# Kernel tuning notes

Hardware: AMD Instinct MI355X
Metric: run time of the kernel (lower is better)

Reference implementation:

```python
import jax, jax.numpy as jnp
import numpy as np

N_NODES = 100000
N_EDGES = 1600000
D_IN = 128
D_HID = 128
N_CLASS = 10
N_GRAPHS = 512
BN_EPS = 1e-5


def setup_inputs() -> dict:
    key = jax.random.key(0)
    ks = jax.random.split(key, 12)
    x = jax.random.normal(ks[0], (N_NODES, D_IN), dtype=jnp.float32)
    edge_index = jax.random.randint(ks[1], (2, N_EDGES), 0, N_NODES, dtype=jnp.int32)
    idx = jnp.sort(jax.random.randint(ks[2], (N_NODES,), 0, N_GRAPHS, dtype=jnp.int32))
    s = 1.0 / np.sqrt(D_HID)
    W1 = jax.random.uniform(ks[3], (D_IN, D_HID), minval=-s, maxval=s, dtype=jnp.float32)
    b1 = jnp.zeros((D_HID,), jnp.float32)
    W2 = jax.random.uniform(ks[4], (D_HID, D_HID), minval=-s, maxval=s, dtype=jnp.float32)
    b2 = jnp.zeros((D_HID,), jnp.float32)
    W3 = jax.random.uniform(ks[5], (D_HID, D_HID), minval=-s, maxval=s, dtype=jnp.float32)
    b3 = jnp.zeros((D_HID,), jnp.float32)
    W4 = jax.random.uniform(ks[6], (D_HID, N_CLASS), minval=-s, maxval=s, dtype=jnp.float32)
    b4 = jnp.zeros((N_CLASS,), jnp.float32)
    gamma = jnp.ones((D_HID,), jnp.float32)
    beta = jnp.zeros((D_HID,), jnp.float32)
    return {"x": x, "edge_index": edge_index, "idx": idx,
            "W1": W1, "b1": b1, "W2": W2, "b2": b2,
            "W3": W3, "b3": b3, "W4": W4, "b4": b4,
            "gamma": gamma, "beta": beta}


def _agg(h, src, dst):
    # (adj + I) @ h : sum of neighbor features plus self-loop
    return jax.ops.segment_sum(h[src], dst, num_segments=N_NODES) + h


def reference(x, edge_index, idx, W1, b1, W2, b2, W3, b3, W4, b4, gamma, beta):
    src, dst = edge_index[0], edge_index[1]
    z1 = jax.nn.relu(_agg(x, src, dst) @ W1 + b1)          # [N, H] (dropout = identity, eval)
    h = _agg(z1, src, dst) @ W2 + b2                        # [N, H]
    pooled = jax.ops.segment_sum(h, idx, num_segments=N_GRAPHS)  # [G, H] scatter-add readout
    # BatchNorm1d over graph (batch) dimension, training-mode batch stats
    mean = jnp.mean(pooled, axis=0)
    var = jnp.var(pooled, axis=0)
    out = (pooled - mean) * jax.lax.rsqrt(var + BN_EPS) * gamma + beta
    zg = jax.nn.relu(out @ W3 + b3)
    logits = zg @ W4 + b4                                   # [G, C]
    return jax.nn.log_softmax(logits, axis=1)
```

## Files before the change

kernel.cpp:

```cpp
#include <hip/hip_runtime.h>
#include <hip/hip_fp16.h>
#include <math.h>

#define NN 100000
#define NE 1600000
#define DH 128
#define NG 512
#define NC 10
#define NSEG 8
#define SEGN 12500
#define CHE 8192
#define NCH 196
#define MAXDEG 48
#define WPITCH 136

#define NB_HIST (NCH * NSEG)
#define NB_CNT  98
#define NB_GEMM ((NN + 63) / 64)

typedef __attribute__((ext_vector_type(8))) _Float16 f16x8;
typedef __attribute__((ext_vector_type(4))) float f32x4;


__global__ __launch_bounds__(256, 3) void k_build(
    const int* __restrict__ dst, const int* __restrict__ src,
    int* __restrict__ counts, int* __restrict__ csr,
    const int* __restrict__ gidx, int* __restrict__ cnt,
    const float* __restrict__ A, const float* __restrict__ W,
    __half* __restrict__ out) {
    int b = blockIdx.x;
    int t = threadIdx.x;
    if (b < NB_HIST) {
        int seg = b & 7;
        int chunk = b >> 3;
        int lo = seg * SEGN, hi = lo + SEGN;
        int e0 = chunk * CHE;
        int e1 = e0 + CHE < NE ? e0 + CHE : NE;
        for (int e = e0 + t * 4; e < e1; e += 1024) {
            int4 d4 = *(const int4*)(dst + e);
            bool i0 = d4.x >= lo && d4.x < hi;
            bool i1 = d4.y >= lo && d4.y < hi;
            bool i2 = d4.z >= lo && d4.z < hi;
            bool i3 = d4.w >= lo && d4.w < hi;
            int4 s4 = {0, 0, 0, 0};
            if (i0 | i1 | i2 | i3) s4 = *(const int4*)(src + e);
            if (i0) {
                int p = atomicAdd(&counts[d4.x], 1);
                if (p < MAXDEG) csr[d4.x * MAXDEG + p] = s4.x;
            }
            if (i1) {
                int p = atomicAdd(&counts[d4.y], 1);
                if (p < MAXDEG) csr[d4.y * MAXDEG + p] = s4.y;
            }
            if (i2) {
                int p = atomicAdd(&counts[d4.z], 1);
                if (p < MAXDEG) csr[d4.z * MAXDEG + p] = s4.z;
            }
            if (i3) {
                int p = atomicAdd(&counts[d4.w], 1);
                if (p < MAXDEG) csr[d4.w * MAXDEG + p] = s4.w;
            }
        }
    } else if (b < NB_HIST + NB_CNT) {
        int cb = b - NB_HIST;
        int n0 = cb * 1024 + t * 4;
        if (n0 >= NN) return;
        int g = gidx[n0];
        int run = 1;
        for (int j = 1; j < 4; ++j) {
            int n = n0 + j;
            if (n < NN) {
                int gg = gidx[n];
                if (gg == g) {
                    run++;
                } else {
                    atomicAdd(&cnt[g], run);
                    g = gg;
                    run = 1;
                }
            }
        }
        atomicAdd(&cnt[g], run);
    } else {
        __shared__ _Float16 sWT[DH * WPITCH];
        __shared__ __align__(16) _Float16 sOut[4][16][DH];
        int gb = b - (NB_HIST + NB_CNT);
        int wv = t >> 6;
        int lane = t & 63;
        for (int i = t; i < DH * DH; i += 256) {
            int k = i >> 7, n = i & 127;
            sWT[n * WPITCH + k] = (_Float16)W[i];
        }
        __syncthreads();

        int m = lane & 15;
        int quad = lane >> 4;
        int node0 = gb * 64 + wv * 16;
        int nodeA = node0 + m;
        if (nodeA >= NN) nodeA = NN - 1;
        const float* arow = A + (size_t)nodeA * DH;

        f16x8 afrag[4];
#pragma unroll
        for (int kt = 0; kt < 4; ++kt) {
            int k0 = kt * 32 + quad * 8;
            float4 u0 = *(const float4*)(arow + k0);
            float4 u1 = *(const float4*)(arow + k0 + 4);
            afrag[kt][0] = (_Float16)u0.x; afrag[kt][1] = (_Float16)u0.y;
            afrag[kt][2] = (_Float16)u0.z; afrag[kt][3] = (_Float16)u0.w;
            afrag[kt][4] = (_Float16)u1.x; afrag[kt][5] = (_Float16)u1.y;
            afrag[kt][6] = (_Float16)u1.z; afrag[kt][7] = (_Float16)u1.w;
        }

#pragma unroll
        for (int ct = 0; ct < 8; ++ct) {
            f32x4 acc = {0.f, 0.f, 0.f, 0.f};
            int n = ct * 16 + m;
#pragma unroll
            for (int kt = 0; kt < 4; ++kt) {
                int k0 = kt * 32 + quad * 8;
                f16x8 bfrag = *(const f16x8*)&sWT[n * WPITCH + k0];
                acc = __builtin_amdgcn_mfma_f32_16x16x32_f16(afrag[kt], bfrag, acc, 0, 0, 0);
            }
#pragma unroll
            for (int r = 0; r < 4; ++r)
                sOut[wv][quad * 4 + r][ct * 16 + m] = (_Float16)acc[r];
        }
        __syncthreads();

        const uint4* so = (const uint4*)&sOut[wv][0][0];
        for (int i = lane; i < 256; i += 64) {
            int row = i >> 4;
            int node = node0 + row;
            if (node < NN) ((uint4*)out)[(size_t)node * 16 + (i & 15)] = so[i];
        }
    }
}


__device__ __forceinline__ void acc8(float* a, const uint4& v, float m) {
    float2 f;
    f = __half22float2(*(const __half2*)&v.x); a[0] = fmaf(m, f.x, a[0]); a[1] = fmaf(m, f.y, a[1]);
    f = __half22float2(*(const __half2*)&v.y); a[2] = fmaf(m, f.x, a[2]); a[3] = fmaf(m, f.y, a[3]);
    f = __half22float2(*(const __half2*)&v.z); a[4] = fmaf(m, f.x, a[4]); a[5] = fmaf(m, f.y, a[5]);
    f = __half22float2(*(const __half2*)&v.w); a[6] = fmaf(m, f.x, a[6]); a[7] = fmaf(m, f.y, a[7]);
}


__global__ __launch_bounds__(256, 4) void k_agg_h(
    const __half* __restrict__ in, const int* __restrict__ counts,
    const int* __restrict__ csr, const float* __restrict__ bias,
    __half* __restrict__ outA) {
    int t = threadIdx.x;
    int lane = t & 15;
    int node = blockIdx.x * 16 + (t >> 4);
    const uint4* in4 = (const uint4*)in;
    float a[8];
#pragma unroll
    for (int j = 0; j < 8; ++j) a[j] = 0.f;
    uint4 sv = in4[(size_t)node * 16 + lane];
    acc8(a, sv, 1.f);
    int e0 = node * MAXDEG;
    int deg = counts[node];
    deg = deg < MAXDEG ? deg : MAXDEG;
    int e1 = e0 + deg;
    int elast = e1 - 1;
    for (int e = e0; e < e1; e += 8) {
        int idx[8];
        float m[8];
#pragma unroll
        for (int i = 0; i < 8; ++i) {
            int ei = e + i;
            int ec = ei < elast ? ei : elast;
            idx[i] = csr[ec];
            m[i] = (ei < e1) ? 1.f : 0.f;
        }
        uint4 v[8];
#pragma unroll
        for (int i = 0; i < 8; ++i) v[i] = in4[(size_t)idx[i] * 16 + lane];
#pragma unroll
        for (int i = 0; i < 8; ++i) acc8(a, v[i], m[i]);
    }
    float4 b0 = ((const float4*)bias)[lane * 2];
    float4 b1v = ((const float4*)bias)[lane * 2 + 1];
    a[0] = fmaxf(a[0] + b0.x, 0.f);  a[1] = fmaxf(a[1] + b0.y, 0.f);
    a[2] = fmaxf(a[2] + b0.z, 0.f);  a[3] = fmaxf(a[3] + b0.w, 0.f);
    a[4] = fmaxf(a[4] + b1v.x, 0.f); a[5] = fmaxf(a[5] + b1v.y, 0.f);
    a[6] = fmaxf(a[6] + b1v.z, 0.f); a[7] = fmaxf(a[7] + b1v.w, 0.f);
    uint4 o;
    *(__half2*)&o.x = __floats2half2_rn(a[0], a[1]);
    *(__half2*)&o.y = __floats2half2_rn(a[2], a[3]);
    *(__half2*)&o.z = __floats2half2_rn(a[4], a[5]);
    *(__half2*)&o.w = __floats2half2_rn(a[6], a[7]);
    ((uint4*)outA)[(size_t)node * 16 + lane] = o;
}


__global__ __launch_bounds__(256, 4) void k_agg_pool_h(
    const __half* __restrict__ in, const int* __restrict__ counts,
    const int* __restrict__ csr, const int* __restrict__ gidx,
    float* __restrict__ pp8) {
    __shared__ __align__(16) float sA[16][DH];
    int t = threadIdx.x;
    int lane = t & 15;
    int p = t >> 4;
    int node0 = blockIdx.x * 16;
    int node = node0 + p;
    const uint4* in4 = (const uint4*)in;
    float a[8];
#pragma unroll
    for (int j = 0; j < 8; ++j) a[j] = 0.f;
    uint4 sv = in4[(size_t)node * 16 + lane];
    acc8(a, sv, 1.f);
    int e0 = node * MAXDEG;
    int deg = counts[node];
    deg = deg < MAXDEG ? deg : MAXDEG;
    int e1 = e0 + deg;
    int elast = e1 - 1;
    for (int e = e0; e < e1; e += 8) {
        int idx[8];
        float m[8];
#pragma unroll
        for (int i = 0; i < 8; ++i) {
            int ei = e + i;
            int ec = ei < elast ? ei : elast;
            idx[i] = csr[ec];
            m[i] = (ei < e1) ? 1.f : 0.f;
        }
        uint4 v[8];
#pragma unroll
        for (int i = 0; i < 8; ++i) v[i] = in4[(size_t)idx[i] * 16 + lane];
#pragma unroll
        for (int i = 0; i < 8; ++i) acc8(a, v[i], m[i]);
    }
    float4* row = (float4*)&sA[p][lane * 8];
    row[0] = make_float4(a[0], a[1], a[2], a[3]);
    row[1] = make_float4(a[4], a[5], a[6], a[7]);
    __syncthreads();
    if (t < DH) {
        float* pp = pp8 + (size_t)(blockIdx.x & 7) * NG * DH;
        int gprev = gidx[node0];
        float run = 0.f;
        for (int q = 0; q < 16; ++q) {
            int g = gidx[node0 + q];
            if (g != gprev) {
                atomicAdd(&pp[gprev * DH + t], run);
                run = 0.f;
                gprev = g;
            }
            run += sA[q][t];
        }
        atomicAdd(&pp[gprev * DH + t], run);
    }
}


__device__ __forceinline__ void fma4(float4& acc, float s, const float4& wv) {
    acc.x = fmaf(s, wv.x, acc.x);
    acc.y = fmaf(s, wv.y, acc.y);
    acc.z = fmaf(s, wv.z, acc.z);
    acc.w = fmaf(s, wv.w, acc.w);
}


__global__ __launch_bounds__(256, 2) void k_pool_mm(
    const float* __restrict__ pp8, const float* __restrict__ W,
    const float* __restrict__ bias, const int* __restrict__ cnt,
    float* __restrict__ pooled) {
    __shared__ __align__(16) float sW[DH * DH];
    __shared__ __align__(16) float sA[32 * DH];
    int t = threadIdx.x;
    int g0 = blockIdx.x * 32;
    {
        const float4* W4g = (const float4*)W;
        float4* sW4 = (float4*)sW;
        for (int i = t; i < DH * DH / 4; i += 256) sW4[i] = W4g[i];
        const float4* P4 = (const float4*)pp8;
        float4* sA4 = (float4*)sA;
        for (int i = t; i < 32 * DH / 4; i += 256) {
            float4 s;
            s.x = 0.f; s.y = 0.f; s.z = 0.f; s.w = 0.f;
#pragma unroll
            for (int c = 0; c < NSEG; ++c) {
                float4 v = P4[(size_t)c * NG * DH / 4 + (size_t)g0 * DH / 4 + i];
                s.x += v.x; s.y += v.y; s.z += v.z; s.w += v.w;
            }
            sA4[i] = s;
        }
    }
    __syncthreads();

    int c4 = t & 31;
    int n0 = (t >> 5) * 4;
    const float4* sA4 = (const float4*)sA;
    const float4* sW4 = (const float4*)sW;
    float4 acc0, acc1, acc2, acc3;
    acc0.x = acc0.y = acc0.z = acc0.w = 0.f;
    acc1 = acc0; acc2 = acc0; acc3 = acc0;

#pragma unroll 2
    for (int kc = 0; kc < DH / 4; ++kc) {
        float4 a0 = sA4[(n0 + 0) * 32 + kc];
        float4 a1 = sA4[(n0 + 1) * 32 + kc];
        float4 a2 = sA4[(n0 + 2) * 32 + kc];
        float4 a3 = sA4[(n0 + 3) * 32 + kc];
        float4 w0 = sW4[(4 * kc + 0) * 32 + c4];
        float4 w1 = sW4[(4 * kc + 1) * 32 + c4];
        float4 w2 = sW4[(4 * kc + 2) * 32 + c4];
        float4 w3 = sW4[(4 * kc + 3) * 32 + c4];
        fma4(acc0, a0.x, w0); fma4(acc0, a0.y, w1); fma4(acc0, a0.z, w2); fma4(acc0, a0.w, w3);
        fma4(acc1, a1.x, w0); fma4(acc1, a1.y, w1); fma4(acc1, a1.z, w2); fma4(acc1, a1.w, w3);
        fma4(acc2, a2.x, w0); fma4(acc2, a2.y, w1); fma4(acc2, a2.z, w2); fma4(acc2, a2.w, w3);
        fma4(acc3, a3.x, w0); fma4(acc3, a3.y, w1); fma4(acc3, a3.z, w2); fma4(acc3, a3.w, w3);
    }

    float4 b2v = ((const float4*)bias)[c4];
    float c0 = (float)cnt[g0 + n0 + 0];
    float c1 = (float)cnt[g0 + n0 + 1];
    float c2 = (float)cnt[g0 + n0 + 2];
    float c3 = (float)cnt[g0 + n0 + 3];
    fma4(acc0, c0, b2v);
    fma4(acc1, c1, b2v);
    fma4(acc2, c2, b2v);
    fma4(acc3, c3, b2v);

    float4* out4 = (float4*)pooled;
    out4[(size_t)(g0 + n0 + 0) * 32 + c4] = acc0;
    out4[(size_t)(g0 + n0 + 1) * 32 + c4] = acc1;
    out4[(size_t)(g0 + n0 + 2) * 32 + c4] = acc2;
    out4[(size_t)(g0 + n0 + 3) * 32 + c4] = acc3;
}


__global__ void k_bnstats(const float* __restrict__ pooled, float* __restrict__ mean,
                          float* __restrict__ rstd) {
    int c = blockIdx.x;
    int l = threadIdx.x;
    float s = 0.f, s2 = 0.f;
    for (int g = l; g < NG; g += 64) {
        float v = pooled[g * DH + c];
        s += v;
        s2 += v * v;
    }
#pragma unroll
    for (int off = 32; off > 0; off >>= 1) {
        s += __shfl_down(s, off, 64);
        s2 += __shfl_down(s2, off, 64);
    }
    if (l == 0) {
        float m = s * (1.f / NG);
        float var = s2 * (1.f / NG) - m * m;
        mean[c] = m;
        rstd[c] = rsqrtf(var + 1e-5f);
    }
}


__global__ __launch_bounds__(128) void k_tail(
    const float* __restrict__ pooled, const float* __restrict__ mean,
    const float* __restrict__ rstd, const float* __restrict__ gamma,
    const float* __restrict__ beta, const float* __restrict__ W3,
    const float* __restrict__ b3, const float* __restrict__ W4,
    const float* __restrict__ b4, float* __restrict__ out) {
    __shared__ __align__(16) float sW[DH * DH];
    __shared__ float sg[DH];
    __shared__ float sz[DH];
    __shared__ float slog[NC];
    __shared__ float slse;
    int g = blockIdx.x, t = threadIdx.x;
    {
        const float4* W34 = (const float4*)W3;
        float4* sW4 = (float4*)sW;
        for (int i = t; i < DH * DH / 4; i += 128) sW4[i] = W34[i];
    }
    float v = pooled[g * DH + t];
    v = (v - mean[t]) * rstd[t] * gamma[t] + beta[t];
    sg[t] = v;
    __syncthreads();
    float acc = b3[t];
#pragma unroll 4
    for (int k = 0; k < DH; ++k) acc = fmaf(sg[k], sW[k * DH + t], acc);
    sz[t] = fmaxf(acc, 0.f);
    __syncthreads();
    if (t < NC) {
        float a = b4[t];
        for (int k = 0; k < DH; ++k) a = fmaf(sz[k], W4[k * NC + t], a);
        slog[t] = a;
    }
    __syncthreads();
    if (t == 0) {
        float mx = slog[0];
        for (int j = 1; j < NC; ++j) mx = fmaxf(mx, slog[j]);
        float se = 0.f;
        for (int j = 0; j < NC; ++j) se += expf(slog[j] - mx);
        slse = mx + logf(se);
    }
    __syncthreads();
    if (t < NC) out[g * NC + t] = slog[t] - slse;
}


extern "C" void kernel_launch(void* const* d_in, const int* in_sizes, int n_in,
                              void* d_out, int out_size, void* d_ws, size_t ws_size,
                              hipStream_t stream) {
    const float* x = (const float*)d_in[0];
    const int* ei = (const int*)d_in[1];
    const int* src = ei;
    const int* dst = ei + NE;
    const int* gidx = (const int*)d_in[2];
    const float* W1 = (const float*)d_in[3];
    const float* b1 = (const float*)d_in[4];
    const float* W2 = (const float*)d_in[5];
    const float* b2 = (const float*)d_in[6];
    const float* W3 = (const float*)d_in[7];
    const float* b3 = (const float*)d_in[8];
    const float* W4 = (const float*)d_in[9];
    const float* b4 = (const float*)d_in[10];
    const float* gamma = (const float*)d_in[11];
    const float* beta = (const float*)d_in[12];
    float* out = (float*)d_out;

    char* w = (char*)d_ws;
    auto take = [&](size_t bytes) {
        char* p = w;
        w += (bytes + 255) & ~size_t(255);
        return p;
    };
    int* counts = (int*)take((size_t)NN * 4);
    int* cnt = (int*)take((size_t)NG * 4);
    float* pp8 = (float*)take((size_t)NSEG * NG * DH * 4);
    size_t zero_bytes = (size_t)((char*)(pp8 + (size_t)NSEG * NG * DH) - (char*)counts);
    int* csr = (int*)take((size_t)NN * MAXDEG * 4);
    __half* y = (__half*)take((size_t)NN * DH * 2);
    __half* z1 = (__half*)take((size_t)NN * DH * 2);
    float* pooled = (float*)take((size_t)NG * DH * 4);
    float* meanb = (float*)take(DH * 4);
    float* rstdb = (float*)take(DH * 4);

    hipMemsetAsync(counts, 0, zero_bytes, stream);

    k_build<<<NB_HIST + NB_CNT + NB_GEMM, 256, 0, stream>>>(
        dst, src, counts, csr, gidx, cnt, x, W1, y);

    k_agg_h<<<NN / 16, 256, 0, stream>>>(y, counts, csr, b1, z1);

    k_agg_pool_h<<<NN / 16, 256, 0, stream>>>(z1, counts, csr, gidx, pp8);
    k_pool_mm<<<NG / 32, 256, 0, stream>>>(pp8, W2, b2, cnt, pooled);

    k_bnstats<<<DH, 64, 0, stream>>>(pooled, meanb, rstdb);
    k_tail<<<NG, 128, 0, stream>>>(pooled, meanb, rstdb, gamma, beta, W3, b3, W4, b4, out);
}
```

Baseline: 360.9 us.

## Store GEMM output in permuted column layout, swizzle weight LDS, drop sOut staging

The first-layer GEMM in k_build now keeps eight accumulators per wave and writes each lane's results straight to global memory in a permuted column order, which removes the sOut LDS staging buffer and its barrier. The permutation is undone downstream: the bias read in k_agg_h is reindexed and the rows of W2 are permuted when k_pool_mm loads them. The transposed weight tile in LDS uses an XOR swizzle instead of padding to avoid bank conflicts. Edge and activation reads use nontemporal loads, and the occupancy hint for k_build is raised, which risks register pressure.

```diff
diff --git a/kernel.cpp b/kernel.cpp
--- a/kernel.cpp
+++ b/kernel.cpp
@@ -12,17 +12,18 @@
 #define CHE 8192
 #define NCH 196
 #define MAXDEG 48
-#define WPITCH 136
 
 #define NB_HIST (NCH * NSEG)
 #define NB_CNT  98
 #define NB_GEMM ((NN + 63) / 64)
 
+
 typedef __attribute__((ext_vector_type(8))) _Float16 f16x8;
 typedef __attribute__((ext_vector_type(4))) float f32x4;
-
-
-__global__ __launch_bounds__(256, 3) void k_build(
+typedef __attribute__((ext_vector_type(4))) int i32x4;
+
+
+__global__ __launch_bounds__(256, 4) void k_build(
     const int* __restrict__ dst, const int* __restrict__ src,
     int* __restrict__ counts, int* __restrict__ csr,
     const int* __restrict__ gidx, int* __restrict__ cnt,
@@ -37,13 +38,14 @@
         int e0 = chunk * CHE;
         int e1 = e0 + CHE < NE ? e0 + CHE : NE;
         for (int e = e0 + t * 4; e < e1; e += 1024) {
-            int4 d4 = *(const int4*)(dst + e);
+            i32x4 d4 = __builtin_nontemporal_load((const i32x4*)(dst + e));
             bool i0 = d4.x >= lo && d4.x < hi;
             bool i1 = d4.y >= lo && d4.y < hi;
             bool i2 = d4.z >= lo && d4.z < hi;
             bool i3 = d4.w >= lo && d4.w < hi;
-            int4 s4 = {0, 0, 0, 0};
-            if (i0 | i1 | i2 | i3) s4 = *(const int4*)(src + e);
+            i32x4 s4 = {0, 0, 0, 0};
+            if (i0 | i1 | i2 | i3)
+                s4 = __builtin_nontemporal_load((const i32x4*)(src + e));
             if (i0) {
                 int p = atomicAdd(&counts[d4.x], 1);
                 if (p < MAXDEG) csr[d4.x * MAXDEG + p] = s4.x;
@@ -82,14 +84,13 @@
         }
         atomicAdd(&cnt[g], run);
     } else {
-        __shared__ _Float16 sWT[DH * WPITCH];
-        __shared__ __align__(16) _Float16 sOut[4][16][DH];
+        __shared__ _Float16 sWT[DH * 128];
         int gb = b - (NB_HIST + NB_CNT);
         int wv = t >> 6;
         int lane = t & 63;
         for (int i = t; i < DH * DH; i += 256) {
             int k = i >> 7, n = i & 127;
-            sWT[n * WPITCH + k] = (_Float16)W[i];
+            sWT[n * 128 + (((k >> 3) ^ (n & 15)) * 8) + (k & 7)] = (_Float16)W[i];
         }
         __syncthreads();
 
@@ -104,35 +105,42 @@
 #pragma unroll
         for (int kt = 0; kt < 4; ++kt) {
             int k0 = kt * 32 + quad * 8;
-            float4 u0 = *(const float4*)(arow + k0);
-            float4 u1 = *(const float4*)(arow + k0 + 4);
+            f32x4 u0 = __builtin_nontemporal_load((const f32x4*)(arow + k0));
+            f32x4 u1 = __builtin_nontemporal_load((const f32x4*)(arow + k0 + 4));
             afrag[kt][0] = (_Float16)u0.x; afrag[kt][1] = (_Float16)u0.y;
             afrag[kt][2] = (_Float16)u0.z; afrag[kt][3] = (_Float16)u0.w;
             afrag[kt][4] = (_Float16)u1.x; afrag[kt][5] = (_Float16)u1.y;
             afrag[kt][6] = (_Float16)u1.z; afrag[kt][7] = (_Float16)u1.w;
         }
 
-#pragma unroll
-        for (int ct = 0; ct < 8; ++ct) {
-            f32x4 acc = {0.f, 0.f, 0.f, 0.f};
-            int n = ct * 16 + m;
-#pragma unroll
-            for (int kt = 0; kt < 4; ++kt) {
-                int k0 = kt * 32 + quad * 8;
-                f16x8 bfrag = *(const f16x8*)&sWT[n * WPITCH + k0];
-                acc = __builtin_amdgcn_mfma_f32_16x16x32_f16(afrag[kt], bfrag, acc, 0, 0, 0);
-            }
-#pragma unroll
-            for (int r = 0; r < 4; ++r)
-                sOut[wv][quad * 4 + r][ct * 16 + m] = (_Float16)acc[r];
-        }
-        __syncthreads();
-
-        const uint4* so = (const uint4*)&sOut[wv][0][0];
-        for (int i = lane; i < 256; i += 64) {
-            int row = i >> 4;
-            int node = node0 + row;
-            if (node < NN) ((uint4*)out)[(size_t)node * 16 + (i & 15)] = so[i];
+        f32x4 acc0 = {0.f, 0.f, 0.f, 0.f};
+        f32x4 acc1 = acc0, acc2 = acc0, acc3 = acc0;
+        f32x4 acc4 = acc0, acc5 = acc0, acc6 = acc0, acc7 = acc0;
+#pragma unroll
+        for (int kt = 0; kt < 4; ++kt) {
+            int kb = kt * 4 + quad;
+            const _Float16* wbase = &sWT[(size_t)m * 128 + ((kb ^ m) * 8)];
+            acc0 = __builtin_amdgcn_mfma_f32_16x16x32_f16(afrag[kt], *(const f16x8*)(wbase + 0 * 16 * 128), acc0, 0, 0, 0);
+            acc1 = __builtin_amdgcn_mfma_f32_16x16x32_f16(afrag[kt], *(const f16x8*)(wbase + 1 * 16 * 128), acc1, 0, 0, 0);
+            acc2 = __builtin_amdgcn_mfma_f32_16x16x32_f16(afrag[kt], *(const f16x8*)(wbase + 2 * 16 * 128), acc2, 0, 0, 0);
+            acc3 = __builtin_amdgcn_mfma_f32_16x16x32_f16(afrag[kt], *(const f16x8*)(wbase + 3 * 16 * 128), acc3, 0, 0, 0);
+            acc4 = __builtin_amdgcn_mfma_f32_16x16x32_f16(afrag[kt], *(const f16x8*)(wbase + 4 * 16 * 128), acc4, 0, 0, 0);
+            acc5 = __builtin_amdgcn_mfma_f32_16x16x32_f16(afrag[kt], *(const f16x8*)(wbase + 5 * 16 * 128), acc5, 0, 0, 0);
+            acc6 = __builtin_amdgcn_mfma_f32_16x16x32_f16(afrag[kt], *(const f16x8*)(wbase + 6 * 16 * 128), acc6, 0, 0, 0);
+            acc7 = __builtin_amdgcn_mfma_f32_16x16x32_f16(afrag[kt], *(const f16x8*)(wbase + 7 * 16 * 128), acc7, 0, 0, 0);
+        }
+
+#pragma unroll
+        for (int r = 0; r < 4; ++r) {
+            int node = node0 + quad * 4 + r;
+            if (node < NN) {
+                uint4 o;
+                *(__half2*)&o.x = __floats2half2_rn(acc0[r], acc1[r]);
+                *(__half2*)&o.y = __floats2half2_rn(acc2[r], acc3[r]);
+                *(__half2*)&o.z = __floats2half2_rn(acc4[r], acc5[r]);
+                *(__half2*)&o.w = __floats2half2_rn(acc6[r], acc7[r]);
+                ((uint4*)out)[(size_t)node * 16 + m] = o;
+            }
         }
     }
 }
@@ -181,12 +189,11 @@
 #pragma unroll
         for (int i = 0; i < 8; ++i) acc8(a, v[i], m[i]);
     }
-    float4 b0 = ((const float4*)bias)[lane * 2];
-    float4 b1v = ((const float4*)bias)[lane * 2 + 1];
-    a[0] = fmaxf(a[0] + b0.x, 0.f);  a[1] = fmaxf(a[1] + b0.y, 0.f);
-    a[2] = fmaxf(a[2] + b0.z, 0.f);  a[3] = fmaxf(a[3] + b0.w, 0.f);
-    a[4] = fmaxf(a[4] + b1v.x, 0.f); a[5] = fmaxf(a[5] + b1v.y, 0.f);
-    a[6] = fmaxf(a[6] + b1v.z, 0.f); a[7] = fmaxf(a[7] + b1v.w, 0.f);
+    float bj[8];
+#pragma unroll
+    for (int j = 0; j < 8; ++j) bj[j] = bias[j * 16 + lane];
+#pragma unroll
+    for (int j = 0; j < 8; ++j) a[j] = fmaxf(a[j] + bj[j], 0.f);
     uint4 o;
     *(__half2*)&o.x = __floats2half2_rn(a[0], a[1]);
     *(__half2*)&o.y = __floats2half2_rn(a[2], a[3]);
@@ -274,7 +281,11 @@
     {
         const float4* W4g = (const float4*)W;
         float4* sW4 = (float4*)sW;
-        for (int i = t; i < DH * DH / 4; i += 256) sW4[i] = W4g[i];
+        for (int i = t; i < DH * DH / 4; i += 256) {
+            int r = i >> 5;
+            int orig = ((r & 7) << 4) + (r >> 3);
+            sW4[i] = W4g[orig * 32 + (i & 31)];
+        }
         const float4* P4 = (const float4*)pp8;
         float4* sA4 = (float4*)sA;
         for (int i = t; i < 32 * DH / 4; i += 256) {
```

Result: no change. 358.5 us (-0.6%).
